# Optimization experiments

Measured on AMD Instinct MI355X. Metric: run time of the kernel, lower is better.

The kernel has to match this reference:

```python
import jax, jax.numpy as jnp
import numpy as np

DT_RANK = 64
D_STATE = 16


def setup_inputs() -> dict:
    key = jax.random.key(0)
    ks = jax.random.split(key, 6)
    B, L, Di = 2, 2048, 2048
    x = jax.random.normal(ks[0], (B, L, Di), dtype=jnp.float32)
    W_xproj = jax.random.normal(ks[1], (DT_RANK + 2 * D_STATE, Di), dtype=jnp.float32) * (Di ** -0.5)
    W_dt = jax.random.uniform(ks[2], (Di, DT_RANK), dtype=jnp.float32, minval=-(DT_RANK ** -0.5), maxval=DT_RANK ** -0.5)
    dt = jnp.exp(jax.random.uniform(ks[3], (Di,), dtype=jnp.float32) * (np.log(0.1) - np.log(0.001)) + np.log(0.001))
    b_dt = dt + jnp.log(-jnp.expm1(-dt))
    A_log = jnp.log(jnp.broadcast_to(jnp.arange(1, D_STATE + 1, dtype=jnp.float32), (Di, D_STATE)))
    D_param = jnp.ones((Di,), dtype=jnp.float32)
    return {"x": x, "W_xproj": W_xproj, "W_dt": W_dt, "b_dt": b_dt, "A_log": A_log, "D_param": D_param}


def _selective_scan(u, delta, A, Bm, Cm):
    # u, delta: (b, l, d); A: (d, n); Bm, Cm: (b, l, n)
    deltaA = jnp.exp(delta[..., None] * A[None, None])          # (b, l, d, n)
    deltaB_u = delta[..., None] * Bm[:, :, None, :] * u[..., None]  # (b, l, d, n)

    def step(h, inp):
        dA, dBu, c = inp                      # dA,dBu: (b,d,n); c: (b,n)
        h = dA * h + dBu
        y = jnp.einsum('bdn,bn->bd', h, c)
        return h, y

    b, l, d = u.shape
    h0 = jnp.zeros((b, d, A.shape[1]), dtype=u.dtype)
    xs = (jnp.moveaxis(deltaA, 1, 0), jnp.moveaxis(deltaB_u, 1, 0), jnp.moveaxis(Cm, 1, 0))
    _, ys = jax.lax.scan(step, h0, xs)        # ys: (l, b, d)
    return jnp.moveaxis(ys, 0, 1)


def reference(x, W_xproj, W_dt, b_dt, A_log, D_param):
    x_dbl = jnp.einsum('bld,ed->ble', x, W_xproj)  # (b, l, dt_rank + 2*n)
    dlt = x_dbl[..., :DT_RANK]
    Bm = x_dbl[..., DT_RANK:DT_RANK + D_STATE]
    Cm = x_dbl[..., DT_RANK + D_STATE:]
    delta = jax.nn.softplus(jnp.einsum('blr,dr->bld', dlt, W_dt) + b_dt)
    A = -jnp.exp(A_log.astype(jnp.float32))
    y = _selective_scan(x, delta, A, Bm, Cm)
    return y + x * D_param[None, None, :]
```

## Files before the change

kernel.cpp:

```cpp
#include <hip/hip_runtime.h>

#define BATCH 2
#define L_SEQ 2048
#define DI 2048
#define NROW (BATCH * L_SEQ)
#define E_DIM 96
#define RNK 64
#define NST 16
#define NCH 64
#define CL 32
#define SPLITK 16
#define KSL (DI / SPLITK)

#define WS_XDBL 0
#define WS_PART 393216
#define WS_HLOC 393216
#define WS_DSUM (393216 + 4194304)

__device__ __forceinline__ float softplusf(float z) {
    return fmaxf(z, 0.f) + log1pf(__expf(-fabsf(z)));
}

__global__ __launch_bounds__(128) void gemm_xproj_part(const float* __restrict__ x,
                                                       const float* __restrict__ Wx,
                                                       float* __restrict__ part) {
    __shared__ float xs[32][65];
    __shared__ float wsh[32][97];
    const int tid = threadIdx.x;
    const int r0 = blockIdx.x * 64;
    const int kbase0 = blockIdx.y * KSL;
    const int rg = tid >> 4;
    const int cg = tid & 15;

    float acc[8][6];
#pragma unroll
    for (int i = 0; i < 8; i++)
#pragma unroll
        for (int j = 0; j < 6; j++) acc[i][j] = 0.f;

    for (int kt = 0; kt < KSL / 32; kt++) {
        const int kb = kbase0 + kt * 32;
#pragma unroll
        for (int rep = 0; rep < 4; rep++) {
            int i = rep * 128 + tid;
            int row = i >> 3;
            int kq = i & 7;
            float4 v = *(const float4*)&x[(long)(r0 + row) * DI + kb + kq * 4];
            xs[kq * 4 + 0][row] = v.x;
            xs[kq * 4 + 1][row] = v.y;
            xs[kq * 4 + 2][row] = v.z;
            xs[kq * 4 + 3][row] = v.w;
        }
#pragma unroll
        for (int rep = 0; rep < 6; rep++) {
            int i = rep * 128 + tid;
            int e = i >> 3;
            int kq = i & 7;
            float4 v = *(const float4*)&Wx[(long)e * DI + kb + kq * 4];
            wsh[kq * 4 + 0][e] = v.x;
            wsh[kq * 4 + 1][e] = v.y;
            wsh[kq * 4 + 2][e] = v.z;
            wsh[kq * 4 + 3][e] = v.w;
        }
        __syncthreads();
#pragma unroll 4
        for (int k = 0; k < 32; k++) {
            float xr[8], wr[6];
#pragma unroll
            for (int i = 0; i < 8; i++) xr[i] = xs[k][rg * 8 + i];
#pragma unroll
            for (int j = 0; j < 6; j++) wr[j] = wsh[k][cg * 6 + j];
#pragma unroll
            for (int i = 0; i < 8; i++)
#pragma unroll
                for (int j = 0; j < 6; j++) acc[i][j] = fmaf(xr[i], wr[j], acc[i][j]);
        }
        __syncthreads();
    }
    const long sbase = (long)blockIdx.y * NROW * E_DIM;
#pragma unroll
    for (int i = 0; i < 8; i++) {
        long rowb = sbase + (long)(r0 + rg * 8 + i) * E_DIM + cg * 6;
#pragma unroll
        for (int j = 0; j < 6; j++) part[rowb + j] = acc[i][j];
    }
}

__global__ __launch_bounds__(256) void xproj_reduce(const float* __restrict__ part,
                                                    float* __restrict__ xdbl) {
    const int i4 = blockIdx.x * 256 + threadIdx.x;
    const float4* p4 = (const float4*)part;
    float4 s = p4[i4];
#pragma unroll
    for (int sp = 1; sp < SPLITK; sp++) {
        float4 v = p4[(long)sp * (NROW * E_DIM / 4) + i4];
        s.x += v.x; s.y += v.y; s.z += v.z; s.w += v.w;
    }
    ((float4*)xdbl)[i4] = s;
}

__global__ __launch_bounds__(256) void gemm_dt(const float* __restrict__ xdbl,
                                               const float* __restrict__ Wdt,
                                               const float* __restrict__ b_dt,
                                               float* __restrict__ delta) {
    __shared__ float dl[32][129];
    __shared__ float wt[32][129];
    const int tid = threadIdx.x;
    const int row0 = blockIdx.x * 128;
    const int d0 = blockIdx.y * 128;
    const int rg = tid >> 4;
    const int cg = tid & 15;

    float acc[8][8];
#pragma unroll
    for (int i = 0; i < 8; i++)
#pragma unroll
        for (int j = 0; j < 8; j++) acc[i][j] = 0.f;

    for (int kt = 0; kt < 2; kt++) {
        const int kb = kt * 32;
#pragma unroll
        for (int rep = 0; rep < 4; rep++) {
            int i = rep * 256 + tid;
            int row = i >> 3;
            int kq = i & 7;
            float4 v = *(const float4*)&xdbl[(long)(row0 + row) * E_DIM + kb + kq * 4];
            dl[kq * 4 + 0][row] = v.x;
            dl[kq * 4 + 1][row] = v.y;
            dl[kq * 4 + 2][row] = v.z;
            dl[kq * 4 + 3][row] = v.w;
        }
#pragma unroll
        for (int rep = 0; rep < 4; rep++) {
            int i = rep * 256 + tid;
            int dd = i >> 3;
            int kq = i & 7;
            float4 v = *(const float4*)&Wdt[(long)(d0 + dd) * RNK + kb + kq * 4];
            wt[kq * 4 + 0][dd] = v.x;
            wt[kq * 4 + 1][dd] = v.y;
            wt[kq * 4 + 2][dd] = v.z;
            wt[kq * 4 + 3][dd] = v.w;
        }
        __syncthreads();
#pragma unroll 4
        for (int k = 0; k < 32; k++) {
            float xr[8], wr[8];
#pragma unroll
            for (int i = 0; i < 8; i++) xr[i] = dl[k][rg * 8 + i];
#pragma unroll
            for (int j = 0; j < 8; j++) wr[j] = wt[k][cg * 8 + j];
#pragma unroll
            for (int i = 0; i < 8; i++)
#pragma unroll
                for (int j = 0; j < 8; j++) acc[i][j] = fmaf(xr[i], wr[j], acc[i][j]);
        }
        __syncthreads();
    }

    float4 b0 = *(const float4*)&b_dt[d0 + cg * 8];
    float4 b1 = *(const float4*)&b_dt[d0 + cg * 8 + 4];
#pragma unroll
    for (int i = 0; i < 8; i++) {
        int row = row0 + rg * 8 + i;
        float4 o0, o1;
        o0.x = softplusf(acc[i][0] + b0.x);
        o0.y = softplusf(acc[i][1] + b0.y);
        o0.z = softplusf(acc[i][2] + b0.z);
        o0.w = softplusf(acc[i][3] + b0.w);
        o1.x = softplusf(acc[i][4] + b1.x);
        o1.y = softplusf(acc[i][5] + b1.y);
        o1.z = softplusf(acc[i][6] + b1.z);
        o1.w = softplusf(acc[i][7] + b1.w);
        *(float4*)&delta[(long)row * DI + d0 + cg * 8] = o0;
        *(float4*)&delta[(long)row * DI + d0 + cg * 8 + 4] = o1;
    }
}

__global__ __launch_bounds__(256) void scan_carry(const float* __restrict__ x,
                                                  const float* __restrict__ delta,
                                                  const float* __restrict__ xdbl,
                                                  const float* __restrict__ A_log,
                                                  float* __restrict__ hloc,
                                                  float* __restrict__ dsumb) {
    __shared__ float bm[CL * NST];
    const int tid = threadIdx.x;
    const int d = blockIdx.x * 256 + tid;
    const int c = blockIdx.y;
    const int b = blockIdx.z;
    const int row0 = b * L_SEQ + c * CL;

    for (int i = tid; i < CL * NST; i += 256) {
        int ll = i >> 4, n = i & 15;
        bm[i] = xdbl[(long)(row0 + ll) * E_DIM + 64 + n];
    }
    __syncthreads();

    float A[16];
#pragma unroll
    for (int q = 0; q < 4; q++) {
        float4 v = *(const float4*)&A_log[(long)d * NST + q * 4];
        A[q * 4 + 0] = -__expf(v.x);
        A[q * 4 + 1] = -__expf(v.y);
        A[q * 4 + 2] = -__expf(v.z);
        A[q * 4 + 3] = -__expf(v.w);
    }
    float h[16];
#pragma unroll
    for (int n = 0; n < 16; n++) h[n] = 0.f;
    float dsum = 0.f;

    long idx = (long)row0 * DI + d;
    float dn = delta[idx], xn = x[idx];
    for (int ll = 0; ll < CL; ll++) {
        float dc = dn, xc = xn;
        long nidx = (ll + 1 < CL) ? idx + DI : idx;
        dn = delta[nidx];
        xn = x[nidx];
        float du = dc * xc;
        float bl[16];
#pragma unroll
        for (int q = 0; q < 4; q++) {
            float4 v = *(const float4*)&bm[ll * NST + q * 4];
            bl[q * 4 + 0] = v.x; bl[q * 4 + 1] = v.y; bl[q * 4 + 2] = v.z; bl[q * 4 + 3] = v.w;
        }
#pragma unroll
        for (int n = 0; n < 16; n++)
            h[n] = fmaf(__expf(dc * A[n]), h[n], du * bl[n]);
        dsum += dc;
        idx += DI;
    }

    const long cb = ((long)(b * NCH + c) * DI + d);
#pragma unroll
    for (int q = 0; q < 4; q++)
        *(float4*)&hloc[cb * 16 + q * 4] =
            make_float4(h[q * 4], h[q * 4 + 1], h[q * 4 + 2], h[q * 4 + 3]);
    dsumb[cb] = dsum;
}

__global__ __launch_bounds__(256) void scan_prefix(const float* __restrict__ A_log,
                                                   float* __restrict__ hloc,
                                                   const float* __restrict__ dsumb) {
    const int g = blockIdx.x * 256 + threadIdx.x;
    const int n = g & 15;
    const int d = (g >> 4) & (DI - 1);
    const int b = g >> 15;
    const float An = -__expf(A_log[(long)d * NST + n]);
    float hc = 0.f;
    for (int c = 0; c < NCH; c++) {
        const long cb = ((long)(b * NCH + c) * DI + d);
        float hl = hloc[cb * 16 + n];
        float dsv = dsumb[cb];
        hloc[cb * 16 + n] = hc;
        hc = fmaf(__expf(An * dsv), hc, hl);
    }
}

__global__ __launch_bounds__(256) void scan_out(const float* __restrict__ x,
                                                const float* __restrict__ xdbl,
                                                const float* __restrict__ A_log,
                                                const float* __restrict__ Dp,
                                                const float* __restrict__ hloc,
                                                float* out) {
    __shared__ float bm[CL * NST];
    __shared__ float cm[CL * NST];
    const int tid = threadIdx.x;
    const int d = blockIdx.x * 256 + tid;
    const int c = blockIdx.y;
    const int b = blockIdx.z;
    const int row0 = b * L_SEQ + c * CL;

    for (int i = tid; i < CL * NST; i += 256) {
        int ll = i >> 4, n = i & 15;
        bm[i] = xdbl[(long)(row0 + ll) * E_DIM + 64 + n];
        cm[i] = xdbl[(long)(row0 + ll) * E_DIM + 80 + n];
    }
    __syncthreads();

    float A[16];
#pragma unroll
    for (int q = 0; q < 4; q++) {
        float4 v = *(const float4*)&A_log[(long)d * NST + q * 4];
        A[q * 4 + 0] = -__expf(v.x);
        A[q * 4 + 1] = -__expf(v.y);
        A[q * 4 + 2] = -__expf(v.z);
        A[q * 4 + 3] = -__expf(v.w);
    }
    float h[16];
    const long cb = ((long)(b * NCH + c) * DI + d);
#pragma unroll
    for (int q = 0; q < 4; q++) {
        float4 v = *(const float4*)&hloc[cb * 16 + q * 4];
        h[q * 4 + 0] = v.x; h[q * 4 + 1] = v.y; h[q * 4 + 2] = v.z; h[q * 4 + 3] = v.w;
    }
    const float Dd = Dp[d];

    long idx = (long)row0 * DI + d;
    float dn = out[idx], xn = x[idx];
    for (int ll = 0; ll < CL; ll++) {
        float dc = dn, xc = xn;
        long nidx = (ll + 1 < CL) ? idx + DI : idx;
        dn = out[nidx];
        xn = x[nidx];
        float du = dc * xc;
        float bl[16], clv[16];
#pragma unroll
        for (int q = 0; q < 4; q++) {
            float4 v = *(const float4*)&bm[ll * NST + q * 4];
            bl[q * 4 + 0] = v.x; bl[q * 4 + 1] = v.y; bl[q * 4 + 2] = v.z; bl[q * 4 + 3] = v.w;
            float4 w = *(const float4*)&cm[ll * NST + q * 4];
            clv[q * 4 + 0] = w.x; clv[q * 4 + 1] = w.y; clv[q * 4 + 2] = w.z; clv[q * 4 + 3] = w.w;
        }
        float y = 0.f;
#pragma unroll
        for (int n = 0; n < 16; n++) {
            h[n] = fmaf(__expf(dc * A[n]), h[n], du * bl[n]);
            y = fmaf(h[n], clv[n], y);
        }
        out[idx] = fmaf(xc, Dd, y);
        idx += DI;
    }
}

extern "C" void kernel_launch(void* const* d_in, const int* in_sizes, int n_in,
                              void* d_out, int out_size, void* d_ws, size_t ws_size,
                              hipStream_t stream) {
    const float* x    = (const float*)d_in[0];
    const float* Wx   = (const float*)d_in[1];
    const float* Wdt  = (const float*)d_in[2];
    const float* bdt  = (const float*)d_in[3];
    const float* Alog = (const float*)d_in[4];
    const float* Dp   = (const float*)d_in[5];
    float* out = (float*)d_out;
    float* ws = (float*)d_ws;
    float* xdbl  = ws + WS_XDBL;
    float* partb = ws + WS_PART;
    float* hloc  = ws + WS_HLOC;
    float* dsumb = ws + WS_DSUM;

    gemm_xproj_part<<<dim3(NROW / 64, SPLITK), 128, 0, stream>>>(x, Wx, partb);
    xproj_reduce<<<dim3(NROW * E_DIM / 4 / 256), 256, 0, stream>>>(partb, xdbl);
    gemm_dt<<<dim3(NROW / 128, DI / 128), 256, 0, stream>>>(xdbl, Wdt, bdt, out);
    scan_carry<<<dim3(DI / 256, NCH, BATCH), 256, 0, stream>>>(x, out, xdbl, Alog, hloc, dsumb);
    scan_prefix<<<dim3(BATCH * DI * NST / 256), 256, 0, stream>>>(Alog, hloc, dsumb);
    scan_out<<<dim3(DI / 256, NCH, BATCH), 256, 0, stream>>>(x, xdbl, Alog, Dp, hloc, out);
}
```

Baseline: 229.5 us.

## Fuse dt projection and softplus into scan carry pass; widen xproj GEMM blocks

Removes the separate gemm_dt kernel. Each scan_carry thread now keeps its 64-wide W_dt row in registers and computes delta on the fly from the dt-rank slice of x_dbl staged in shared memory, writing delta out for the later output pass. This drops one launch and one full read of the delta tensor. The cost is 64 extra registers per thread and the dt dot product done serially inside the scan loop. Separately, the x-projection GEMM moves to 256 threads with 4x6 tiles per thread and padded shared-memory rows, trading per-thread reuse for more threads.

New measurement: 223.3 us. -2.7%, faster.

```diff
diff --git a/kernel.cpp b/kernel.cpp
--- a/kernel.cpp
+++ b/kernel.cpp
@@ -21,28 +21,28 @@
     return fmaxf(z, 0.f) + log1pf(__expf(-fabsf(z)));
 }
 
-__global__ __launch_bounds__(128) void gemm_xproj_part(const float* __restrict__ x,
+__global__ __launch_bounds__(256) void gemm_xproj_part(const float* __restrict__ x,
                                                        const float* __restrict__ Wx,
                                                        float* __restrict__ part) {
-    __shared__ float xs[32][65];
-    __shared__ float wsh[32][97];
+    __shared__ float xs[32][68];
+    __shared__ float wsh[32][100];
     const int tid = threadIdx.x;
     const int r0 = blockIdx.x * 64;
     const int kbase0 = blockIdx.y * KSL;
     const int rg = tid >> 4;
     const int cg = tid & 15;
 
-    float acc[8][6];
-#pragma unroll
-    for (int i = 0; i < 8; i++)
+    float acc[4][6];
+#pragma unroll
+    for (int i = 0; i < 4; i++)
 #pragma unroll
         for (int j = 0; j < 6; j++) acc[i][j] = 0.f;
 
     for (int kt = 0; kt < KSL / 32; kt++) {
         const int kb = kbase0 + kt * 32;
 #pragma unroll
-        for (int rep = 0; rep < 4; rep++) {
-            int i = rep * 128 + tid;
+        for (int rep = 0; rep < 2; rep++) {
+            int i = rep * 256 + tid;
             int row = i >> 3;
             int kq = i & 7;
             float4 v = *(const float4*)&x[(long)(r0 + row) * DI + kb + kq * 4];
@@ -52,8 +52,8 @@
             xs[kq * 4 + 3][row] = v.w;
         }
 #pragma unroll
-        for (int rep = 0; rep < 6; rep++) {
-            int i = rep * 128 + tid;
+        for (int rep = 0; rep < 3; rep++) {
+            int i = rep * 256 + tid;
             int e = i >> 3;
             int kq = i & 7;
             float4 v = *(const float4*)&Wx[(long)e * DI + kb + kq * 4];
@@ -63,15 +63,15 @@
             wsh[kq * 4 + 3][e] = v.w;
         }
         __syncthreads();
-#pragma unroll 4
+#pragma unroll 8
         for (int k = 0; k < 32; k++) {
-            float xr[8], wr[6];
-#pragma unroll
-            for (int i = 0; i < 8; i++) xr[i] = xs[k][rg * 8 + i];
+            float xr[4], wr[6];
+#pragma unroll
+            for (int i = 0; i < 4; i++) xr[i] = xs[k][rg * 4 + i];
 #pragma unroll
             for (int j = 0; j < 6; j++) wr[j] = wsh[k][cg * 6 + j];
 #pragma unroll
-            for (int i = 0; i < 8; i++)
+            for (int i = 0; i < 4; i++)
 #pragma unroll
                 for (int j = 0; j < 6; j++) acc[i][j] = fmaf(xr[i], wr[j], acc[i][j]);
         }
@@ -79,8 +79,8 @@
     }
     const long sbase = (long)blockIdx.y * NROW * E_DIM;
 #pragma unroll
-    for (int i = 0; i < 8; i++) {
-        long rowb = sbase + (long)(r0 + rg * 8 + i) * E_DIM + cg * 6;
+    for (int i = 0; i < 4; i++) {
+        long rowb = sbase + (long)(r0 + rg * 4 + i) * E_DIM + cg * 6;
 #pragma unroll
         for (int j = 0; j < 6; j++) part[rowb + j] = acc[i][j];
     }
@@ -99,89 +99,15 @@
     ((float4*)xdbl)[i4] = s;
 }
 
-__global__ __launch_bounds__(256) void gemm_dt(const float* __restrict__ xdbl,
-                                               const float* __restrict__ Wdt,
-                                               const float* __restrict__ b_dt,
-                                               float* __restrict__ delta) {
-    __shared__ float dl[32][129];
-    __shared__ float wt[32][129];
-    const int tid = threadIdx.x;
-    const int row0 = blockIdx.x * 128;
-    const int d0 = blockIdx.y * 128;
-    const int rg = tid >> 4;
-    const int cg = tid & 15;
-
-    float acc[8][8];
-#pragma unroll
-    for (int i = 0; i < 8; i++)
-#pragma unroll
-        for (int j = 0; j < 8; j++) acc[i][j] = 0.f;
-
-    for (int kt = 0; kt < 2; kt++) {
-        const int kb = kt * 32;
-#pragma unroll
-        for (int rep = 0; rep < 4; rep++) {
-            int i = rep * 256 + tid;
-            int row = i >> 3;
-            int kq = i & 7;
-            float4 v = *(const float4*)&xdbl[(long)(row0 + row) * E_DIM + kb + kq * 4];
-            dl[kq * 4 + 0][row] = v.x;
-            dl[kq * 4 + 1][row] = v.y;
-            dl[kq * 4 + 2][row] = v.z;
-            dl[kq * 4 + 3][row] = v.w;
-        }
-#pragma unroll
-        for (int rep = 0; rep < 4; rep++) {
-            int i = rep * 256 + tid;
-            int dd = i >> 3;
-            int kq = i & 7;
-            float4 v = *(const float4*)&Wdt[(long)(d0 + dd) * RNK + kb + kq * 4];
-            wt[kq * 4 + 0][dd] = v.x;
-            wt[kq * 4 + 1][dd] = v.y;
-            wt[kq * 4 + 2][dd] = v.z;
-            wt[kq * 4 + 3][dd] = v.w;
-        }
-        __syncthreads();
-#pragma unroll 4
-        for (int k = 0; k < 32; k++) {
-            float xr[8], wr[8];
-#pragma unroll
-            for (int i = 0; i < 8; i++) xr[i] = dl[k][rg * 8 + i];
-#pragma unroll
-            for (int j = 0; j < 8; j++) wr[j] = wt[k][cg * 8 + j];
-#pragma unroll
-            for (int i = 0; i < 8; i++)
-#pragma unroll
-                for (int j = 0; j < 8; j++) acc[i][j] = fmaf(xr[i], wr[j], acc[i][j]);
-        }
-        __syncthreads();
-    }
-
-    float4 b0 = *(const float4*)&b_dt[d0 + cg * 8];
-    float4 b1 = *(const float4*)&b_dt[d0 + cg * 8 + 4];
-#pragma unroll
-    for (int i = 0; i < 8; i++) {
-        int row = row0 + rg * 8 + i;
-        float4 o0, o1;
-        o0.x = softplusf(acc[i][0] + b0.x);
-        o0.y = softplusf(acc[i][1] + b0.y);
-        o0.z = softplusf(acc[i][2] + b0.z);
-        o0.w = softplusf(acc[i][3] + b0.w);
-        o1.x = softplusf(acc[i][4] + b1.x);
-        o1.y = softplusf(acc[i][5] + b1.y);
-        o1.z = softplusf(acc[i][6] + b1.z);
-        o1.w = softplusf(acc[i][7] + b1.w);
-        *(float4*)&delta[(long)row * DI + d0 + cg * 8] = o0;
-        *(float4*)&delta[(long)row * DI + d0 + cg * 8 + 4] = o1;
-    }
-}
-
-__global__ __launch_bounds__(256) void scan_carry(const float* __restrict__ x,
-                                                  const float* __restrict__ delta,
-                                                  const float* __restrict__ xdbl,
-                                                  const float* __restrict__ A_log,
-                                                  float* __restrict__ hloc,
-                                                  float* __restrict__ dsumb) {
+__global__ __launch_bounds__(256) void scan_carry_fused(const float* __restrict__ x,
+                                                        const float* __restrict__ xdbl,
+                                                        const float* __restrict__ Wdt,
+                                                        const float* __restrict__ bdt,
+                                                        const float* __restrict__ A_log,
+                                                        float* __restrict__ delta_out,
+                                                        float* __restrict__ hloc,
+                                                        float* __restrict__ dsumb) {
+    __shared__ float dlt_s[CL][RNK];
     __shared__ float bm[CL * NST];
     const int tid = threadIdx.x;
     const int d = blockIdx.x * 256 + tid;
@@ -189,11 +115,29 @@
     const int b = blockIdx.z;
     const int row0 = b * L_SEQ + c * CL;
 
-    for (int i = tid; i < CL * NST; i += 256) {
-        int ll = i >> 4, n = i & 15;
-        bm[i] = xdbl[(long)(row0 + ll) * E_DIM + 64 + n];
+    for (int j = tid; j < CL * 20; j += 256) {
+        int row = j / 20, q = j % 20;
+        float4 v = *(const float4*)&xdbl[(long)(row0 + row) * E_DIM + q * 4];
+        if (q < 16) {
+            *(float4*)&dlt_s[row][q * 4] = v;
+        } else {
+            int n = (q - 16) * 4;
+            bm[row * NST + n + 0] = v.x;
+            bm[row * NST + n + 1] = v.y;
+            bm[row * NST + n + 2] = v.z;
+            bm[row * NST + n + 3] = v.w;
+        }
     }
     __syncthreads();
+
+    float wdtr[64];
+#pragma unroll
+    for (int q = 0; q < 16; q++) {
+        float4 v = *(const float4*)&Wdt[(long)d * RNK + q * 4];
+        wdtr[q * 4 + 0] = v.x; wdtr[q * 4 + 1] = v.y;
+        wdtr[q * 4 + 2] = v.z; wdtr[q * 4 + 3] = v.w;
+    }
+    const float bd = bdt[d];
 
     float A[16];
 #pragma unroll
@@ -210,12 +154,21 @@
     float dsum = 0.f;
 
     long idx = (long)row0 * DI + d;
-    float dn = delta[idx], xn = x[idx];
+    float xn = x[idx];
     for (int ll = 0; ll < CL; ll++) {
-        float dc = dn, xc = xn;
-        long nidx = (ll + 1 < CL) ? idx + DI : idx;
-        dn = delta[nidx];
-        xn = x[nidx];
+        float xc = xn;
+        if (ll + 1 < CL) xn = x[idx + DI];
+        float dv = bd;
+#pragma unroll
+        for (int q = 0; q < 16; q++) {
+            float4 s = *(const float4*)&dlt_s[ll][q * 4];
+            dv = fmaf(s.x, wdtr[q * 4 + 0], dv);
+            dv = fmaf(s.y, wdtr[q * 4 + 1], dv);
+            dv = fmaf(s.z, wdtr[q * 4 + 2], dv);
+            dv = fmaf(s.w, wdtr[q * 4 + 3], dv);
+        }
+        float dc = softplusf(dv);
+        delta_out[idx] = dc;
         float du = dc * xc;
         float bl[16];
 #pragma unroll
@@ -338,10 +291,10 @@
     float* hloc  = ws + WS_HLOC;
     float* dsumb = ws + WS_DSUM;
 
-    gemm_xproj_part<<<dim3(NROW / 64, SPLITK), 128, 0, stream>>>(x, Wx, partb);
+    gemm_xproj_part<<<dim3(NROW / 64, SPLITK), 256, 0, stream>>>(x, Wx, partb);
     xproj_reduce<<<dim3(NROW * E_DIM / 4 / 256), 256, 0, stream>>>(partb, xdbl);
-    gemm_dt<<<dim3(NROW / 128, DI / 128), 256, 0, stream>>>(xdbl, Wdt, bdt, out);
-    scan_carry<<<dim3(DI / 256, NCH, BATCH), 256, 0, stream>>>(x, out, xdbl, Alog, hloc, dsumb);
+    scan_carry_fused<<<dim3(DI / 256, NCH, BATCH), 256, 0, stream>>>(x, xdbl, Wdt, bdt,
+                                                                     Alog, out, hloc, dsumb);
     scan_prefix<<<dim3(BATCH * DI * NST / 256), 256, 0, stream>>>(Alog, hloc, dsumb);
     scan_out<<<dim3(DI / 256, NCH, BATCH), 256, 0, stream>>>(x, xdbl, Alog, Dp, hloc, out);
 }
```
